# Optimization experiments

Measured on AMD Instinct MI355X. Metric: run time of the kernel, lower is better.

## Reference

```python
import jax, jax.numpy as jnp
import numpy as np

EPS = 1e-5
N0, K1, K2 = 1000, 500, 100  # node counts fixed by the view() calls in the source


def _conv_bn_relu(x, w, b, g, be):
    # Conv1d(k=1) == per-node linear; BatchNorm1d in training mode over nodes
    h = x @ w.T + b                      # (N, Cout)
    mu = h.mean(0)
    var = h.var(0)                       # biased variance, as torch BN uses
    return jax.nn.relu(g * (h - mu) * jax.lax.rsqrt(var + EPS) + be)


def _linear_relu(x, w, b):
    return jax.nn.relu(x @ w.T + b)


def _sag_pool(x, src, dst, ew, w_rel, w_root, bias, k):
    # SAGPooling with GraphConv scorer (sum aggregation weighted by edge_attr)
    N = x.shape[0]
    agg = jax.ops.segment_sum(ew[:, None] * x[src], dst, num_segments=N)  # (N, C)
    score = agg @ w_rel + x @ w_root + bias                               # (N,)
    top_s, perm = jax.lax.top_k(score, k)
    xk = x[perm] * jnp.tanh(top_s)[:, None]                               # (k, C)
    # re-index edges: keep only edges between surviving nodes (mask, fixed E)
    new_idx = jnp.zeros(N, jnp.int32).at[perm].set(jnp.arange(k, dtype=jnp.int32))
    keep = jnp.zeros(N, bool).at[perm].set(True)
    valid = keep[src] & keep[dst]
    nsrc = jnp.where(valid, new_idx[src], 0)
    ndst = jnp.where(valid, new_idx[dst], 0)
    new_ew = jnp.where(valid, ew, 0.0)  # zero weight == edge removed
    return xk, nsrc, ndst, new_ew


def setup_inputs() -> dict:
    key = jax.random.key(0)
    ks = jax.random.split(key, 32)
    nrm = lambda k, sh, s=0.05: jax.random.normal(k, sh, jnp.float32) * s
    E = 32000
    return {
        "x": jax.random.normal(ks[0], (1, N0, 3), jnp.float32),
        "edge_index": jax.random.randint(ks[1], (2, E), 0, N0, jnp.int32),
        "edge_attr": jax.random.uniform(ks[2], (E,), jnp.float32),
        # input: Conv1d(3,64)+BN
        "w0": nrm(ks[3], (64, 3)), "b0": jnp.zeros(64), "g0": jnp.ones(64), "be0": jnp.zeros(64),
        # mlp_first: Conv1d(64,64)+BN
        "w1": nrm(ks[4], (64, 64)), "b1": jnp.zeros(64), "g1": jnp.ones(64), "be1": jnp.zeros(64),
        # mlp_second: Conv1d(64,128)+BN, Conv1d(128,200)+BN
        "w2a": nrm(ks[5], (128, 64)), "b2a": jnp.zeros(128), "g2a": jnp.ones(128), "be2a": jnp.zeros(128),
        "w2b": nrm(ks[6], (200, 128)), "b2b": jnp.zeros(200), "g2b": jnp.ones(200), "be2b": jnp.zeros(200),
        # mlp_third: Conv1d(200,128), Conv1d(128,2) (no BN)
        "w3a": nrm(ks[7], (128, 200)), "b3a": jnp.zeros(128),
        "w3b": nrm(ks[8], (2, 128)), "b3b": jnp.zeros(2),
        # SAGPooling scorers (GraphConv(in_channels, 1))
        "p1_wrel": nrm(ks[9], (64,)), "p1_wroot": nrm(ks[10], (64,)), "p1_b": jnp.zeros(()),
        "p2_wrel": nrm(ks[11], (200,)), "p2_wroot": nrm(ks[12], (200,)), "p2_b": jnp.zeros(()),
    }


def reference(x, edge_index, edge_attr,
              w0, b0, g0, be0, w1, b1, g1, be1,
              w2a, b2a, g2a, be2a, w2b, b2b, g2b, be2b,
              w3a, b3a, w3b, b3b,
              p1_wrel, p1_wroot, p1_b, p2_wrel, p2_wroot, p2_b):
    h = x.reshape(N0, 3)
    src, dst = edge_index[0], edge_index[1]
    ew = edge_attr.reshape(-1)

    h = _conv_bn_relu(h, w0, b0, g0, be0)      # (1000, 64)
    h = _conv_bn_relu(h, w1, b1, g1, be1)      # (1000, 64)
    h, src, dst, ew = _sag_pool(h, src, dst, ew, p1_wrel, p1_wroot, p1_b, K1)

    h = _conv_bn_relu(h, w2a, b2a, g2a, be2a)  # (500, 128)
    h = _conv_bn_relu(h, w2b, b2b, g2b, be2b)  # (500, 200)
    h, src, dst, ew = _sag_pool(h, src, dst, ew, p2_wrel, p2_wroot, p2_b, K2)

    g = h.max(0)                               # global max pool over 100 nodes -> (200,)
    h3 = _linear_relu(g, w3a, b3a)             # (128,)
    out = _linear_relu(h3, w3b, b3b)           # (2,)
    return jax.nn.log_softmax(out)[None, :]    # (1, 2)
```

## Files before the change

### kernel.cpp

```cpp
#include <hip/hip_runtime.h>
#include <math.h>

#define EPS 1e-5f
#define N0 1000
#define NK1 500
#define NK2 100
#define NE 32000

__device__ __forceinline__ float bnr(float h, float sc, float sh) {
    float v = fmaf(h, sc, sh);
    return v > 0.f ? v : 0.f;
}

__global__ __launch_bounds__(256) void k_lin01(
        const float* __restrict__ x, const float* __restrict__ w0,
        const float* __restrict__ b0, const float* __restrict__ g0,
        const float* __restrict__ be0, const float* __restrict__ w1,
        const float* __restrict__ b1, float* __restrict__ h1,
        float* __restrict__ psum1, float* __restrict__ sc1, float* __restrict__ sc2) {
    __shared__ float xs[16][68], wsm[64][65];
    __shared__ float sc0[64], sh0[64];
    __shared__ float redA[256], redB[256];
    const int b = blockIdx.x, t = threadIdx.x;
    const int c = t & 63, slot = t >> 6;
    const int nb = b * 16;

    int gid = b * 256 + t;
    if (gid < 1000) sc1[gid] = 0.f;
    else if (gid < 1500) sc2[gid - 1000] = 0.f;

    {
        float wa = w0[c * 3], wb_ = w0[c * 3 + 1], wc_ = w0[c * 3 + 2], bb = b0[c];
        float s = 0.f, q = 0.f;
        for (int n = slot; n < N0; n += 4) {
            float h = fmaf(wa, x[n * 3], fmaf(wb_, x[n * 3 + 1], fmaf(wc_, x[n * 3 + 2], bb)));
            s += h; q += h * h;
        }
        redA[t] = s; redB[t] = q;
        __syncthreads();
        if (t < 64) {
            float S = redA[t] + redA[t + 64] + redA[t + 128] + redA[t + 192];
            float Q = redB[t] + redB[t + 64] + redB[t + 128] + redB[t + 192];
            float mu = S * (1.f / N0);
            float var = Q * (1.f / N0) - mu * mu;
            float sv = g0[t] * rsqrtf(var + EPS);
            sc0[t] = sv; sh0[t] = be0[t] - mu * sv;
        }
        __syncthreads();
    }
    for (int i = 0; i < 4; ++i) {
        int e = t + i * 256;
        int r = e >> 6, cc = e & 63;
        int n = nb + r;
        float v = 0.f;
        if (n < N0) {
            float h = fmaf(w0[cc * 3], x[n * 3],
                      fmaf(w0[cc * 3 + 1], x[n * 3 + 1],
                      fmaf(w0[cc * 3 + 2], x[n * 3 + 2], b0[cc])));
            v = bnr(h, sc0[cc], sh0[cc]);
        }
        xs[r][cc] = v;
    }
    for (int i = 0; i < 16; ++i) {
        int e = t + i * 256;
        wsm[e >> 6][e & 63] = w1[e];
    }
    __syncthreads();
    const int r0 = slot * 4;
    float bb1 = b1[c];
    float a0 = bb1, a1 = bb1, a2 = bb1, a3 = bb1;
    #pragma unroll
    for (int kq = 0; kq < 16; ++kq) {
        float w0v = wsm[c][4 * kq],     w1v = wsm[c][4 * kq + 1];
        float w2v = wsm[c][4 * kq + 2], w3v = wsm[c][4 * kq + 3];
        float4 x0 = *(const float4*)&xs[r0 + 0][4 * kq];
        float4 x1 = *(const float4*)&xs[r0 + 1][4 * kq];
        float4 x2 = *(const float4*)&xs[r0 + 2][4 * kq];
        float4 x3 = *(const float4*)&xs[r0 + 3][4 * kq];
        a0 = fmaf(x0.x, w0v, fmaf(x0.y, w1v, fmaf(x0.z, w2v, fmaf(x0.w, w3v, a0))));
        a1 = fmaf(x1.x, w0v, fmaf(x1.y, w1v, fmaf(x1.z, w2v, fmaf(x1.w, w3v, a1))));
        a2 = fmaf(x2.x, w0v, fmaf(x2.y, w1v, fmaf(x2.z, w2v, fmaf(x2.w, w3v, a2))));
        a3 = fmaf(x3.x, w0v, fmaf(x3.y, w1v, fmaf(x3.z, w2v, fmaf(x3.w, w3v, a3))));
    }
    float av[4] = {a0, a1, a2, a3};
    float sacc = 0.f, qacc = 0.f;
    #pragma unroll
    for (int i = 0; i < 4; ++i) {
        int n = nb + r0 + i;
        if (n < N0) {
            h1[n * 64 + c] = av[i];
            sacc += av[i]; qacc += av[i] * av[i];
        }
    }
    __syncthreads();
    redA[t] = sacc; redB[t] = qacc;
    __syncthreads();
    if (t < 64) {
        psum1[b * 128 + t]      = redA[t] + redA[t + 64] + redA[t + 128] + redA[t + 192];
        psum1[b * 128 + 64 + t] = redB[t] + redB[t + 64] + redB[t + 128] + redB[t + 192];
    }
}

__global__ __launch_bounds__(256) void k_pool1scat(
        const float* __restrict__ h1, const float* __restrict__ psum1,
        const float* __restrict__ g1, const float* __restrict__ be1,
        const float* __restrict__ wrel, const float* __restrict__ wroot,
        const float* __restrict__ pb, const int* __restrict__ ei,
        const float* __restrict__ ea, float* __restrict__ sc1) {
    __shared__ float tt[1008], rt[1008], acc[1008];
    __shared__ float bsc[64], bsh[64];
    __shared__ float red[128];
    const int b = blockIdx.x, t = threadIdx.x;
    if (t < 128) {
        float s = 0.f;
        for (int i = 0; i < 64; ++i) s += psum1[i * 128 + t];
        red[t] = s;
    }
    for (int i = t; i < 1008; i += 256) acc[i] = 0.f;
    __syncthreads();
    if (t < 64) {
        float mu = red[t] * (1.f / N0);
        float var = red[64 + t] * (1.f / N0) - mu * mu;
        float sv = g1[t] * rsqrtf(var + EPS);
        bsc[t] = sv; bsh[t] = be1[t] - mu * sv;
    }
    __syncthreads();
    {
        const int sub = t & 3, grp = t >> 2;
        float wrv[16], wov[16], scv[16], shv[16];
        #pragma unroll
        for (int i = 0; i < 16; ++i) {
            int ch = sub * 16 + i;
            wrv[i] = wrel[ch]; wov[i] = wroot[ch];
            scv[i] = bsc[ch];  shv[i] = bsh[ch];
        }
        float pbv = pb[0];
        for (int p = 0; p < 16; ++p) {
            int n = p * 64 + grp;
            if (n < N0) {
                const float* hp = h1 + n * 64 + sub * 16;
                float dr = 0.f, dt = 0.f;
                #pragma unroll
                for (int i = 0; i < 16; ++i) {
                    float v = bnr(hp[i], scv[i], shv[i]);
                    dr = fmaf(v, wrv[i], dr);
                    dt = fmaf(v, wov[i], dt);
                }
                dr += __shfl_xor(dr, 1, 64); dr += __shfl_xor(dr, 2, 64);
                dt += __shfl_xor(dt, 1, 64); dt += __shfl_xor(dt, 2, 64);
                if (sub == 0) { tt[n] = dr; rt[n] = dt + pbv; }
            }
        }
    }
    __syncthreads();
    for (int e = b * 2000 + t; e < b * 2000 + 2000; e += 256) {
        float w = ea[e];
        if (w != 0.f) atomicAdd(&acc[ei[NE + e]], w * tt[ei[e]]);
    }
    __syncthreads();
    {
        int n = b * 63 + t;
        if (t < 63 && n < N0) atomicAdd(&sc1[n], rt[n]);
    }
    for (int i = t; i < N0; i += 256) {
        float v = acc[i];
        if (v != 0.f) atomicAdd(&sc1[i], v);
    }
}

__global__ __launch_bounds__(256) void k_rank1_lin2a(
        const float* __restrict__ h1, const float* __restrict__ psum1,
        const float* __restrict__ g1, const float* __restrict__ be1,
        const float* __restrict__ sc1, const float* __restrict__ w2a,
        const float* __restrict__ b2a, float* __restrict__ h2a,
        float* __restrict__ psum2a, int* __restrict__ rk_g) {
    __shared__ float ss[N0];
    __shared__ float xp[16][68];
    __shared__ float wsm[128][65];
    __shared__ float bsc[64], bsh[64];
    __shared__ float red[256], redq[256];
    __shared__ int rloc[16], svj[16];
    __shared__ float thv[16];
    __shared__ int nsS;
    const int b = blockIdx.x, t = threadIdx.x;
    const int lane = t & 63, wv = t >> 6;
    const int nb = b * 16;
    const int nn = (N0 - nb) < 0 ? 0 : ((N0 - nb) < 16 ? (N0 - nb) : 16);

    for (int i = t; i < N0; i += 256) ss[i] = sc1[i];
    if (t < 128) {
        float s = 0.f;
        for (int i = 0; i < 64; ++i) s += psum1[i * 128 + t];
        red[t] = s;
    }
    __syncthreads();
    if (t < 64) {
        float mu = red[t] * (1.f / N0);
        float var = red[64 + t] * (1.f / N0) - mu * mu;
        float sv = g1[t] * rsqrtf(var + EPS);
        bsc[t] = sv; bsh[t] = be1[t] - mu * sv;
    }
    __syncthreads();
    for (int it = 0; it < 4; ++it) {
        int j = it * 4 + wv;
        int n = nb + j;
        if (j < nn) {
            float s = ss[n];
            int r = 0;
            for (int m = lane; m < N0; m += 64) {
                float x = ss[m];
                r += (x > s) || (x == s && m < n);
            }
            #pragma unroll
            for (int msk = 32; msk >= 1; msk >>= 1) r += __shfl_xor(r, msk, 64);
            if (lane == 0) { rk_g[n] = r; rloc[j] = r; }
        } else if (lane == 0) rloc[j] = 1 << 20;
    }
    __syncthreads();
    if (t == 0) {
        int c_ = 0;
        for (int j = 0; j < 16; ++j)
            if (rloc[j] < NK1) { svj[c_] = j; ++c_; }
        nsS = c_;
    }
    __syncthreads();
    const int ns = nsS;
    if (t < ns) thv[t] = tanhf(ss[nb + svj[t]]);
    __syncthreads();
    for (int e = t; e < 16 * 64; e += 256) {
        int i = e >> 6, c = e & 63;
        xp[i][c] = (i < ns) ? bnr(h1[(nb + svj[i]) * 64 + c], bsc[c], bsh[c]) * thv[i] : 0.f;
    }
    for (int e = t; e < 128 * 64; e += 256)
        wsm[e >> 6][e & 63] = w2a[e];
    __syncthreads();
    const int c2 = t & 127, half = t >> 7;
    float hac[8];
    {
        float bb = b2a[c2];
        #pragma unroll
        for (int i = 0; i < 8; ++i) hac[i] = bb;
    }
    #pragma unroll
    for (int kq = 0; kq < 16; ++kq) {
        float w0v = wsm[c2][4 * kq],     w1v = wsm[c2][4 * kq + 1];
        float w2v = wsm[c2][4 * kq + 2], w3v = wsm[c2][4 * kq + 3];
        #pragma unroll
        for (int i = 0; i < 8; ++i) {
            float4 x4 = *(const float4*)&xp[half * 8 + i][4 * kq];
            hac[i] = fmaf(x4.x, w0v, fmaf(x4.y, w1v, fmaf(x4.z, w2v, fmaf(x4.w, w3v, hac[i]))));
        }
    }
    float s = 0.f, q = 0.f;
    #pragma unroll
    for (int i = 0; i < 8; ++i) {
        int sl = half * 8 + i;
        if (sl < ns) {
            int r = rloc[svj[sl]];
            h2a[r * 128 + c2] = hac[i];
            s += hac[i]; q += hac[i] * hac[i];
        }
    }
    __syncthreads();
    red[t] = s; redq[t] = q;
    __syncthreads();
    if (t < 128) {
        psum2a[b * 256 + t]       = red[t] + red[t + 128];
        psum2a[b * 256 + 128 + t] = redq[t] + redq[t + 128];
    }
}

__global__ __launch_bounds__(256) void k_lin2b(
        const float* __restrict__ h2a, const float* __restrict__ psum2a,
        const float* __restrict__ g2a, const float* __restrict__ be2a,
        const float* __restrict__ w2b, const float* __restrict__ b2b,
        float* __restrict__ h2b, float* __restrict__ psum2b) {
    __shared__ float wsm[200][33];
    __shared__ float xs[8][36];
    __shared__ float sc[128], sh[128];
    __shared__ float red[256];
    const int b = blockIdx.x, t = threadIdx.x;
    const int nb = b * 8;
    const int nrows = (NK1 - nb) < 0 ? 0 : ((NK1 - nb) < 8 ? (NK1 - nb) : 8);
    if (t < 128) {
        float s = 0.f;
        for (int i = 0; i < 64; ++i) s += psum2a[i * 256 + t];
        red[t] = s;
    }
    {
        float s = 0.f;
        if (t >= 128) for (int i = 0; i < 64; ++i) s += psum2a[i * 256 + t];
        __syncthreads();
        if (t >= 128) red[t] = s;
        __syncthreads();
    }
    if (t < 128) {
        float mu = red[t] * (1.f / NK1);
        float var = red[128 + t] * (1.f / NK1) - mu * mu;
        float sv = g2a[t] * rsqrtf(var + EPS);
        sc[t] = sv; sh[t] = be2a[t] - mu * sv;
    }
    float acc[8];
    float bb = (t < 200) ? b2b[t] : 0.f;
    #pragma unroll
    for (int r = 0; r < 8; ++r) acc[r] = bb;
    for (int kt = 0; kt < 4; ++kt) {
        int k0 = kt * 32;
        __syncthreads();
        for (int i = 0; i < 25; ++i) {
            int e = t + i * 256;
            wsm[e >> 5][e & 31] = w2b[(e >> 5) * 128 + k0 + (e & 31)];
        }
        {
            int r = t >> 5, k = t & 31;
            xs[r][k] = (r < nrows)
                ? bnr(h2a[(nb + r) * 128 + k0 + k], sc[k0 + k], sh[k0 + k]) : 0.f;
        }
        __syncthreads();
        if (t < 200) {
            #pragma unroll
            for (int kq = 0; kq < 8; ++kq) {
                float w0v = wsm[t][4 * kq],     w1v = wsm[t][4 * kq + 1];
                float w2v = wsm[t][4 * kq + 2], w3v = wsm[t][4 * kq + 3];
                #pragma unroll
                for (int r = 0; r < 8; ++r) {
                    float4 xv = *(const float4*)&xs[r][4 * kq];
                    acc[r] = fmaf(xv.x, w0v, fmaf(xv.y, w1v, fmaf(xv.z, w2v, fmaf(xv.w, w3v, acc[r]))));
                }
            }
        }
    }
    if (t < 200) {
        float s = 0.f, q = 0.f;
        #pragma unroll
        for (int r = 0; r < 8; ++r) {
            if (r < nrows) {
                h2b[(nb + r) * 200 + t] = acc[r];
                s += acc[r]; q += acc[r] * acc[r];
            }
        }
        psum2b[b * 400 + t]       = s;
        psum2b[b * 400 + 200 + t] = q;
    }
}

__global__ __launch_bounds__(256) void k_pool2scat(
        const float* __restrict__ h2b, const float* __restrict__ psum2b,
        const float* __restrict__ g2b, const float* __restrict__ be2b,
        const float* __restrict__ wrel, const float* __restrict__ wroot,
        const float* __restrict__ pb, const int* __restrict__ ei,
        const float* __restrict__ ea, const int* __restrict__ rk_g,
        float* __restrict__ sc2) {
    __shared__ float tt[512], rt[512], acc[512], tmp[400];
    __shared__ float bsc[200], bsh[200];
    const int b = blockIdx.x, t = threadIdx.x;
    for (int idx = t; idx < 400; idx += 256) {
        float s = 0.f;
        for (int i = 0; i < 64; ++i) s += psum2b[i * 400 + idx];
        tmp[idx] = s;
    }
    for (int i = t; i < 512; i += 256) acc[i] = 0.f;
    __syncthreads();
    if (t < 200) {
        float mu = tmp[t] * (1.f / NK1);
        float var = tmp[200 + t] * (1.f / NK1) - mu * mu;
        float sv = g2b[t] * rsqrtf(var + EPS);
        bsc[t] = sv; bsh[t] = be2b[t] - mu * sv;
    }
    __syncthreads();
    {
        const int sub = t & 3, grp = t >> 2;
        float pbv = pb[0];
        for (int p = 0; p < 8; ++p) {
            int n = p * 64 + grp;
            if (n < NK1) {
                const float* hp = h2b + n * 200 + sub * 50;
                float dr = 0.f, dt = 0.f;
                for (int i = 0; i < 50; ++i) {
                    int ch = sub * 50 + i;
                    float v = bnr(hp[i], bsc[ch], bsh[ch]);
                    dr = fmaf(v, wrel[ch], dr);
                    dt = fmaf(v, wroot[ch], dt);
                }
                dr += __shfl_xor(dr, 1, 64); dr += __shfl_xor(dr, 2, 64);
                dt += __shfl_xor(dt, 1, 64); dt += __shfl_xor(dt, 2, 64);
                if (sub == 0) { tt[n] = dr; rt[n] = dt + pbv; }
            }
        }
    }
    __syncthreads();
    for (int e = b * 2000 + t; e < b * 2000 + 2000; e += 256) {
        float w = ea[e];
        if (w != 0.f) {
            int rs = rk_g[ei[e]], rd = rk_g[ei[NE + e]];
            if (rs < NK1 && rd < NK1) atomicAdd(&acc[rd], w * tt[rs]);
        }
    }
    __syncthreads();
    {
        int n = b * 32 + t;
        if (t < 32 && n < NK1) atomicAdd(&sc2[n], rt[n]);
    }
    for (int i = t; i < NK1; i += 256) {
        float v = acc[i];
        if (v != 0.f) atomicAdd(&sc2[i], v);
    }
}

__global__ __launch_bounds__(1024) void k_final(
        const float* __restrict__ h2b, const float* __restrict__ psum2b,
        const float* __restrict__ g2b, const float* __restrict__ be2b,
        const float* __restrict__ sc2, const float* __restrict__ w3a,
        const float* __restrict__ b3a, const float* __restrict__ w3b,
        const float* __restrict__ b3b, float* __restrict__ out) {
    __shared__ float ss[512], tmp[400];
    __shared__ float bsc[200], bsh[200];
    __shared__ int pn[NK2];
    __shared__ float th[NK2];
    __shared__ float gp[16 * 200];
    __shared__ float g[200], h3[128], o[2];
    const int t = threadIdx.x;
    const int lane = t & 63, wv = t >> 6;

    for (int idx = t; idx < 400; idx += 1024) {
        float s = 0.f;
        for (int i = 0; i < 64; ++i) s += psum2b[i * 400 + idx];
        tmp[idx] = s;
    }
    for (int i = t; i < NK1; i += 1024) ss[i] = sc2[i];
    for (int i = t; i < 16 * 200; i += 1024) gp[i] = -1e30f;
    __syncthreads();
    if (t < 200) {
        float mu = tmp[t] * (1.f / NK1);
        float var = tmp[200 + t] * (1.f / NK1) - mu * mu;
        float sv = g2b[t] * rsqrtf(var + EPS);
        bsc[t] = sv; bsh[t] = be2b[t] - mu * sv;
    }
    __syncthreads();
    if (t < NK1) {
        float s = ss[t];
        int r = 0;
        for (int m = 0; m < NK1; ++m) {
            float x = ss[m];
            r += (x > s) || (x == s && m < t);
        }
        if (r < NK2) { pn[r] = t; th[r] = tanhf(s); }
    }
    __syncthreads();
    for (int j = wv; j < NK2; j += 16) {
        int n = pn[j];
        float tn = th[j];
        #pragma unroll
        for (int jj = 0; jj < 4; ++jj) {
            int ch = lane + 64 * jj;
            if (ch < 200) {
                float v = bnr(h2b[n * 200 + ch], bsc[ch], bsh[ch]) * tn;
                gp[wv * 200 + ch] = fmaxf(gp[wv * 200 + ch], v);
            }
        }
    }
    __syncthreads();
    if (t < 200) {
        float m = gp[t];
        #pragma unroll
        for (int i = 1; i < 16; ++i) m = fmaxf(m, gp[i * 200 + t]);
        g[t] = m;
    }
    __syncthreads();
    for (int r = wv; r < 128; r += 16) {
        float p = 0.f;
        #pragma unroll
        for (int jj = 0; jj < 4; ++jj) {
            int ch = lane + 64 * jj;
            if (ch < 200) p = fmaf(w3a[r * 200 + ch], g[ch], p);
        }
        #pragma unroll
        for (int m = 32; m >= 1; m >>= 1) p += __shfl_xor(p, m, 64);
        if (lane == 0) h3[r] = fmaxf(p + b3a[r], 0.f);
    }
    __syncthreads();
    if (t < 128) {
        int ow = t >> 6;
        float p = w3b[ow * 128 + lane] * h3[lane]
                + w3b[ow * 128 + 64 + lane] * h3[64 + lane];
        #pragma unroll
        for (int m = 32; m >= 1; m >>= 1) p += __shfl_xor(p, m, 64);
        if (lane == 0) o[ow] = fmaxf(p + b3b[ow], 0.f);
    }
    __syncthreads();
    if (t == 0) {
        float m = fmaxf(o[0], o[1]);
        float l = m + logf(expf(o[0] - m) + expf(o[1] - m));
        out[0] = o[0] - l;
        out[1] = o[1] - l;
    }
}

extern "C" void kernel_launch(void* const* d_in, const int* in_sizes, int n_in,
                              void* d_out, int out_size, void* d_ws, size_t ws_size,
                              hipStream_t stream) {
    const float* x    = (const float*)d_in[0];
    const int*   ei   = (const int*)d_in[1];
    const float* ea   = (const float*)d_in[2];
    const float* w0   = (const float*)d_in[3];
    const float* b0   = (const float*)d_in[4];
    const float* g0   = (const float*)d_in[5];
    const float* be0  = (const float*)d_in[6];
    const float* w1   = (const float*)d_in[7];
    const float* b1   = (const float*)d_in[8];
    const float* g1   = (const float*)d_in[9];
    const float* be1  = (const float*)d_in[10];
    const float* w2a  = (const float*)d_in[11];
    const float* b2a  = (const float*)d_in[12];
    const float* g2a  = (const float*)d_in[13];
    const float* be2a = (const float*)d_in[14];
    const float* w2b  = (const float*)d_in[15];
    const float* b2b  = (const float*)d_in[16];
    const float* g2b  = (const float*)d_in[17];
    const float* be2b = (const float*)d_in[18];
    const float* w3a  = (const float*)d_in[19];
    const float* b3a  = (const float*)d_in[20];
    const float* w3b  = (const float*)d_in[21];
    const float* b3b  = (const float*)d_in[22];
    const float* p1_wrel  = (const float*)d_in[23];
    const float* p1_wroot = (const float*)d_in[24];
    const float* p1_b     = (const float*)d_in[25];
    const float* p2_wrel  = (const float*)d_in[26];
    const float* p2_wroot = (const float*)d_in[27];
    const float* p2_b     = (const float*)d_in[28];

    float* ws = (float*)d_ws;
    float* h1     = ws;
    float* h2a    = ws + 64000;
    float* h2b    = ws + 128000;
    float* psum1  = ws + 228000;
    float* psum2a = ws + 236192;
    float* psum2b = ws + 252576;
    float* sc1    = ws + 278176;
    float* sc2    = ws + 279176;
    int*   rk_g   = (int*)(ws + 279676);
    float* out    = (float*)d_out;

    k_lin01<<<64, 256, 0, stream>>>(x, w0, b0, g0, be0, w1, b1, h1, psum1, sc1, sc2);
    k_pool1scat<<<16, 256, 0, stream>>>(h1, psum1, g1, be1, p1_wrel, p1_wroot, p1_b,
                                        ei, ea, sc1);
    k_rank1_lin2a<<<64, 256, 0, stream>>>(h1, psum1, g1, be1, sc1, w2a, b2a,
                                          h2a, psum2a, rk_g);
    k_lin2b<<<64, 256, 0, stream>>>(h2a, psum2a, g2a, be2a, w2b, b2b, h2b, psum2b);
    k_pool2scat<<<16, 256, 0, stream>>>(h2b, psum2b, g2b, be2b, p2_wrel, p2_wroot, p2_b,
                                        ei, ea, rk_g, sc2);
    k_final<<<1, 1024, 0, stream>>>(h2b, psum2b, g2b, be2b, sc2, w3a, b3a, w3b, b3b, out);
}
```

Before: 136.3 us.

## Compute BN0 stats from input moments, transpose partial sums, retile lin2b, parallelize rank

First-layer BatchNorm statistics now come from the 9 first- and second-order moments of the 3-channel input, which replaces a per-channel loop over all 1000 nodes. Partial-sum buffers are stored transposed so the consumers reduce them with contiguous float4 loads instead of strided scalar loads. k_lin2b now processes 16 rows per block over 32 blocks, stages the normalized activations in shared memory and reads weights straight from global. The final kernel's top-k rank uses all waves with a lane-strided count and a shuffle reduction. The moment formula for the variance can lose precision through cancellation, and 32 blocks give lin2b less parallelism.

```diff
diff --git a/kernel.cpp b/kernel.cpp
--- a/kernel.cpp
+++ b/kernel.cpp
@@ -21,8 +21,10 @@
     __shared__ float xs[16][68], wsm[64][65];
     __shared__ float sc0[64], sh0[64];
     __shared__ float redA[256], redB[256];
+    __shared__ float mom[4][9];
     const int b = blockIdx.x, t = threadIdx.x;
     const int c = t & 63, slot = t >> 6;
+    const int lane = t & 63, wv = t >> 6;
     const int nb = b * 16;
 
     int gid = b * 256 + t;
@@ -30,17 +32,40 @@
     else if (gid < 1500) sc2[gid - 1000] = 0.f;
 
     {
-        float wa = w0[c * 3], wb_ = w0[c * 3 + 1], wc_ = w0[c * 3 + 2], bb = b0[c];
-        float s = 0.f, q = 0.f;
-        for (int n = slot; n < N0; n += 4) {
-            float h = fmaf(wa, x[n * 3], fmaf(wb_, x[n * 3 + 1], fmaf(wc_, x[n * 3 + 2], bb)));
-            s += h; q += h * h;
-        }
-        redA[t] = s; redB[t] = q;
+        float mm[9] = {0.f, 0.f, 0.f, 0.f, 0.f, 0.f, 0.f, 0.f, 0.f};
+        for (int n = t; n < N0; n += 256) {
+            float x0 = x[3 * n], x1 = x[3 * n + 1], x2 = x[3 * n + 2];
+            mm[0] += x0; mm[1] += x1; mm[2] += x2;
+            mm[3] += x0 * x0; mm[4] += x1 * x1; mm[5] += x2 * x2;
+            mm[6] += x0 * x1; mm[7] += x0 * x2; mm[8] += x1 * x2;
+        }
+        #pragma unroll
+        for (int k = 0; k < 9; ++k) {
+            #pragma unroll
+            for (int msk = 32; msk >= 1; msk >>= 1) mm[k] += __shfl_xor(mm[k], msk, 64);
+        }
+        if (lane < 9) mom[wv][lane] = mm[lane] * 0.f;
+        if (lane == 0) {
+            #pragma unroll
+            for (int k = 0; k < 9; ++k) mom[wv][k] = mm[k];
+        }
         __syncthreads();
         if (t < 64) {
-            float S = redA[t] + redA[t + 64] + redA[t + 128] + redA[t + 192];
-            float Q = redB[t] + redB[t + 64] + redB[t + 128] + redB[t + 192];
+            float M0 = mom[0][0] + mom[1][0] + mom[2][0] + mom[3][0];
+            float M1 = mom[0][1] + mom[1][1] + mom[2][1] + mom[3][1];
+            float M2 = mom[0][2] + mom[1][2] + mom[2][2] + mom[3][2];
+            float P00 = mom[0][3] + mom[1][3] + mom[2][3] + mom[3][3];
+            float P11 = mom[0][4] + mom[1][4] + mom[2][4] + mom[3][4];
+            float P22 = mom[0][5] + mom[1][5] + mom[2][5] + mom[3][5];
+            float P01 = mom[0][6] + mom[1][6] + mom[2][6] + mom[3][6];
+            float P02 = mom[0][7] + mom[1][7] + mom[2][7] + mom[3][7];
+            float P12 = mom[0][8] + mom[1][8] + mom[2][8] + mom[3][8];
+            float wa = w0[t * 3], wb = w0[t * 3 + 1], wc = w0[t * 3 + 2], bb = b0[t];
+            float lin = wa * M0 + wb * M1 + wc * M2;
+            float S = lin + (float)N0 * bb;
+            float Q = wa * wa * P00 + wb * wb * P11 + wc * wc * P22
+                    + 2.f * (wa * wb * P01 + wa * wc * P02 + wb * wc * P12)
+                    + 2.f * bb * lin + (float)N0 * bb * bb;
             float mu = S * (1.f / N0);
             float var = Q * (1.f / N0) - mu * mu;
             float sv = g0[t] * rsqrtf(var + EPS);
@@ -96,9 +121,30 @@
     redA[t] = sacc; redB[t] = qacc;
     __syncthreads();
     if (t < 64) {
-        psum1[b * 128 + t]      = redA[t] + redA[t + 64] + redA[t + 128] + redA[t + 192];
-        psum1[b * 128 + 64 + t] = redB[t] + redB[t + 64] + redB[t + 128] + redB[t + 192];
-    }
+        psum1[t * 64 + b]        = redA[t] + redA[t + 64] + redA[t + 128] + redA[t + 192];
+        psum1[(64 + t) * 64 + b] = redB[t] + redB[t + 64] + redB[t + 128] + redB[t + 192];
+    }
+}
+
+__device__ __forceinline__ float sum64c(const float* p) {
+    const float4* p4 = (const float4*)p;
+    float4 a = p4[0];
+    #pragma unroll
+    for (int i = 1; i < 16; ++i) {
+        float4 v = p4[i];
+        a.x += v.x; a.y += v.y; a.z += v.z; a.w += v.w;
+    }
+    return (a.x + a.y) + (a.z + a.w);
+}
+__device__ __forceinline__ float sum32c(const float* p) {
+    const float4* p4 = (const float4*)p;
+    float4 a = p4[0];
+    #pragma unroll
+    for (int i = 1; i < 8; ++i) {
+        float4 v = p4[i];
+        a.x += v.x; a.y += v.y; a.z += v.z; a.w += v.w;
+    }
+    return (a.x + a.y) + (a.z + a.w);
 }
 
 __global__ __launch_bounds__(256) void k_pool1scat(
@@ -111,11 +157,7 @@
     __shared__ float bsc[64], bsh[64];
     __shared__ float red[128];
     const int b = blockIdx.x, t = threadIdx.x;
-    if (t < 128) {
-        float s = 0.f;
-        for (int i = 0; i < 64; ++i) s += psum1[i * 128 + t];
-        red[t] = s;
-    }
+    if (t < 128) red[t] = sum64c(psum1 + t * 64);
     for (int i = t; i < 1008; i += 256) acc[i] = 0.f;
     __syncthreads();
     if (t < 64) {
@@ -188,11 +230,7 @@
     const int nn = (N0 - nb) < 0 ? 0 : ((N0 - nb) < 16 ? (N0 - nb) : 16);
 
     for (int i = t; i < N0; i += 256) ss[i] = sc1[i];
-    if (t < 128) {
-        float s = 0.f;
-        for (int i = 0; i < 64; ++i) s += psum1[i * 128 + t];
-        red[t] = s;
-    }
+    if (t < 128) red[t] = sum64c(psum1 + t * 64);
     __syncthreads();
     if (t < 64) {
         float mu = red[t] * (1.f / N0);
@@ -265,8 +303,8 @@
     red[t] = s; redq[t] = q;
     __syncthreads();
     if (t < 128) {
-        psum2a[b * 256 + t]       = red[t] + red[t + 128];
-        psum2a[b * 256 + 128 + t] = redq[t] + redq[t + 128];
+        psum2a[t * 64 + b]         = red[t] + red[t + 128];
+        psum2a[(128 + t) * 64 + b] = redq[t] + redq[t + 128];
     }
 }
 
@@ -275,72 +313,49 @@
         const float* __restrict__ g2a, const float* __restrict__ be2a,
         const float* __restrict__ w2b, const float* __restrict__ b2b,
         float* __restrict__ h2b, float* __restrict__ psum2b) {
-    __shared__ float wsm[200][33];
-    __shared__ float xs[8][36];
+    __shared__ float zL[16][132];
     __shared__ float sc[128], sh[128];
     __shared__ float red[256];
     const int b = blockIdx.x, t = threadIdx.x;
-    const int nb = b * 8;
-    const int nrows = (NK1 - nb) < 0 ? 0 : ((NK1 - nb) < 8 ? (NK1 - nb) : 8);
-    if (t < 128) {
-        float s = 0.f;
-        for (int i = 0; i < 64; ++i) s += psum2a[i * 256 + t];
-        red[t] = s;
-    }
-    {
-        float s = 0.f;
-        if (t >= 128) for (int i = 0; i < 64; ++i) s += psum2a[i * 256 + t];
-        __syncthreads();
-        if (t >= 128) red[t] = s;
-        __syncthreads();
-    }
+    const int nb = b * 16;
+    const int nrows = (NK1 - nb) < 16 ? (NK1 - nb) : 16;
+    if (t < 256) red[t] = sum64c(psum2a + t * 64);
+    __syncthreads();
     if (t < 128) {
         float mu = red[t] * (1.f / NK1);
         float var = red[128 + t] * (1.f / NK1) - mu * mu;
         float sv = g2a[t] * rsqrtf(var + EPS);
         sc[t] = sv; sh[t] = be2a[t] - mu * sv;
     }
-    float acc[8];
-    float bb = (t < 200) ? b2b[t] : 0.f;
-    #pragma unroll
-    for (int r = 0; r < 8; ++r) acc[r] = bb;
-    for (int kt = 0; kt < 4; ++kt) {
-        int k0 = kt * 32;
-        __syncthreads();
-        for (int i = 0; i < 25; ++i) {
-            int e = t + i * 256;
-            wsm[e >> 5][e & 31] = w2b[(e >> 5) * 128 + k0 + (e & 31)];
-        }
-        {
-            int r = t >> 5, k = t & 31;
-            xs[r][k] = (r < nrows)
-                ? bnr(h2a[(nb + r) * 128 + k0 + k], sc[k0 + k], sh[k0 + k]) : 0.f;
-        }
-        __syncthreads();
-        if (t < 200) {
+    __syncthreads();
+    for (int e = t; e < 16 * 128; e += 256) {
+        int r = e >> 7, k = e & 127;
+        zL[r][k] = (r < nrows) ? bnr(h2a[(nb + r) * 128 + k], sc[k], sh[k]) : 0.f;
+    }
+    __syncthreads();
+    if (t < 200) {
+        float acc[16];
+        float bb = b2b[t];
+        #pragma unroll
+        for (int i = 0; i < 16; ++i) acc[i] = bb;
+        for (int kq = 0; kq < 32; ++kq) {
+            float4 w4 = *(const float4*)&w2b[t * 128 + 4 * kq];
             #pragma unroll
-            for (int kq = 0; kq < 8; ++kq) {
-                float w0v = wsm[t][4 * kq],     w1v = wsm[t][4 * kq + 1];
-                float w2v = wsm[t][4 * kq + 2], w3v = wsm[t][4 * kq + 3];
-                #pragma unroll
-                for (int r = 0; r < 8; ++r) {
-                    float4 xv = *(const float4*)&xs[r][4 * kq];
-                    acc[r] = fmaf(xv.x, w0v, fmaf(xv.y, w1v, fmaf(xv.z, w2v, fmaf(xv.w, w3v, acc[r]))));
-                }
+            for (int i = 0; i < 16; ++i) {
+                float4 z4 = *(const float4*)&zL[i][4 * kq];
+                acc[i] = fmaf(z4.x, w4.x, fmaf(z4.y, w4.y, fmaf(z4.z, w4.z, fmaf(z4.w, w4.w, acc[i]))));
             }
         }
-    }
-    if (t < 200) {
         float s = 0.f, q = 0.f;
         #pragma unroll
-        for (int r = 0; r < 8; ++r) {
-            if (r < nrows) {
-                h2b[(nb + r) * 200 + t] = acc[r];
-                s += acc[r]; q += acc[r] * acc[r];
+        for (int i = 0; i < 16; ++i) {
+            if (i < nrows) {
+                h2b[(nb + i) * 200 + t] = acc[i];
+                s += acc[i]; q += acc[i] * acc[i];
             }
         }
-        psum2b[b * 400 + t]       = s;
-        psum2b[b * 400 + 200 + t] = q;
+        psum2b[t * 32 + b]         = s;
+        psum2b[(200 + t) * 32 + b] = q;
     }
 }
 
@@ -354,11 +369,7 @@
     __shared__ float tt[512], rt[512], acc[512], tmp[400];
     __shared__ float bsc[200], bsh[200];
     const int b = blockIdx.x, t = threadIdx.x;
-    for (int idx = t; idx < 400; idx += 256) {
-        float s = 0.f;
-        for (int i = 0; i < 64; ++i) s += psum2b[i * 400 + idx];
-        tmp[idx] = s;
-    }
+    for (int idx = t; idx < 400; idx += 256) tmp[idx] = sum32c(psum2b + idx * 32);
     for (int i = t; i < 512; i += 256) acc[i] = 0.f;
     __syncthreads();
     if (t < 200) {
@@ -422,11 +433,7 @@
     const int t = threadIdx.x;
     const int lane = t & 63, wv = t >> 6;
 
-    for (int idx = t; idx < 400; idx += 1024) {
-        float s = 0.f;
-        for (int i = 0; i < 64; ++i) s += psum2b[i * 400 + idx];
-        tmp[idx] = s;
-    }
+    for (int idx = t; idx < 400; idx += 1024) tmp[idx] = sum32c(psum2b + idx * 32);
     for (int i = t; i < NK1; i += 1024) ss[i] = sc2[i];
     for (int i = t; i < 16 * 200; i += 1024) gp[i] = -1e30f;
     __syncthreads();
@@ -437,14 +444,16 @@
         bsc[t] = sv; bsh[t] = be2b[t] - mu * sv;
     }
     __syncthreads();
-    if (t < NK1) {
-        float s = ss[t];
+    for (int n = wv; n < NK1; n += 16) {
+        float s = ss[n];
         int r = 0;
-        for (int m = 0; m < NK1; ++m) {
+        for (int m = lane; m < NK1; m += 64) {
             float x = ss[m];
-            r += (x > s) || (x == s && m < t);
-        }
-        if (r < NK2) { pn[r] = t; th[r] = tanhf(s); }
+            r += (x > s) || (x == s && m < n);
+        }
+        #pragma unroll
+        for (int msk = 32; msk >= 1; msk >>= 1) r += __shfl_xor(r, msk, 64);
+        if (lane == 0 && r < NK2) { pn[r] = n; th[r] = tanhf(s); }
     }
     __syncthreads();
     for (int j = wv; j < NK2; j += 16) {
@@ -536,9 +545,9 @@
     float* psum1  = ws + 228000;
     float* psum2a = ws + 236192;
     float* psum2b = ws + 252576;
-    float* sc1    = ws + 278176;
-    float* sc2    = ws + 279176;
-    int*   rk_g   = (int*)(ws + 279676);
+    float* sc1    = ws + 265376;
+    float* sc2    = ws + 266376;
+    int*   rk_g   = (int*)(ws + 266876);
     float* out    = (float*)d_out;
 
     k_lin01<<<64, 256, 0, stream>>>(x, w0, b0, g0, be0, w1, b1, h1, psum1, sc1, sc2);
@@ -546,7 +555,7 @@
                                         ei, ea, sc1);
     k_rank1_lin2a<<<64, 256, 0, stream>>>(h1, psum1, g1, be1, sc1, w2a, b2a,
                                           h2a, psum2a, rk_g);
-    k_lin2b<<<64, 256, 0, stream>>>(h2a, psum2a, g2a, be2a, w2b, b2b, h2b, psum2b);
+    k_lin2b<<<32, 256, 0, stream>>>(h2a, psum2a, g2a, be2a, w2b, b2b, h2b, psum2b);
     k_pool2scat<<<16, 256, 0, stream>>>(h2b, psum2b, g2b, be2b, p2_wrel, p2_wroot, p2_b,
                                         ei, ea, rk_g, sc2);
     k_final<<<1, 1024, 0, stream>>>(h2b, psum2b, g2b, be2b, sc2, w3a, b3a, w3b, b3b, out);
```

After: 111.1 us. 18.5% less time.
